# Kernel tuning notes

Hardware: AMD Instinct MI355X
Metric: run time of the kernel (lower is better)

Reference implementation:

```python
import jax, jax.numpy as jnp
import numpy as np

L, B, S, D, H, F, E, G, KG, K = 2, 2, 1024, 1024, 16, 1024, 8, 4, 2, 2
EPS = 1e-5
HD = D // H


def setup_inputs() -> dict:
    key = jax.random.key(0)
    ks = jax.random.split(key, 16)
    def nrm(k, shape):
        return jax.random.normal(k, shape, jnp.float32) * 0.02
    inp = {
        'src': jax.random.normal(ks[0], (B, S, D), jnp.float32),
        'attn_qkv_w': nrm(ks[1], (L, 3 * D, D)), 'attn_qkv_b': jnp.zeros((L, 3 * D), jnp.float32),
        'attn_out_w': nrm(ks[2], (L, D, D)), 'attn_out_b': jnp.zeros((L, D), jnp.float32),
        'norm1_g': jnp.ones((L, D), jnp.float32), 'norm1_b': jnp.zeros((L, D), jnp.float32),
        'norm2_g': jnp.ones((L, D), jnp.float32), 'norm2_b': jnp.zeros((L, D), jnp.float32),
        'gate_w': nrm(ks[3], (L, E, D)),
        'exp_w1': nrm(ks[4], (L, E, F, D)), 'exp_b1': jnp.zeros((L, E, F), jnp.float32),
        'exp_w2': nrm(ks[5], (L, E, D, F)), 'exp_b2': jnp.zeros((L, E, D), jnp.float32),
        'exp_w3': nrm(ks[6], (L, E, F, D)), 'exp_b3': jnp.zeros((L, E, F), jnp.float32),
        'sh_w1': nrm(ks[7], (L, F, D)), 'sh_b1': jnp.zeros((L, F), jnp.float32),
        'sh_w2': nrm(ks[8], (L, D, F)), 'sh_b2': jnp.zeros((L, D), jnp.float32),
        'sh_w3': nrm(ks[9], (L, F, D)), 'sh_b3': jnp.zeros((L, F), jnp.float32),
        'final_g': jnp.ones((D,), jnp.float32), 'final_b': jnp.zeros((D,), jnp.float32),
    }
    return inp


def _ln(x, g, b):
    mu = jnp.mean(x, -1, keepdims=True)
    var = jnp.mean(jnp.square(x - mu), -1, keepdims=True)
    return (x - mu) * jax.lax.rsqrt(var + EPS) * g + b


def _swiglu(x, w1, b1, w2, b2, w3, b3):
    return (jax.nn.silu(x @ w1.T + b1) * (x @ w3.T + b3)) @ w2.T + b2


def _attn(h, wqkv, bqkv, wo, bo):
    qkv = h @ wqkv.T + bqkv                       # (B,S,3D)
    q, k, v = jnp.split(qkv, 3, axis=-1)
    sp = lambda t: t.reshape(B, S, H, HD).transpose(0, 2, 1, 3)
    q, k, v = sp(q), sp(k), sp(v)
    sc = jnp.einsum('bhqd,bhkd->bhqk', q, k) / np.sqrt(HD).astype(np.float32)
    causal = jnp.tril(jnp.ones((S, S), bool))
    sc = jnp.where(causal, sc, -jnp.inf)
    a = jax.nn.softmax(sc, axis=-1)
    o = jnp.einsum('bhqk,bhkd->bhqd', a, v).transpose(0, 2, 1, 3).reshape(B, S, D)
    return o @ wo.T + bo


def _moe(x, gw, w1, b1, w2, b2, w3, b3, sw1, sb1, sw2, sb2, sw3, sb3):
    # x: (T,D) flattened tokens
    T = x.shape[0]
    scores = jax.nn.softmax(x @ gw.T, axis=-1)    # (T,E)
    orig = scores
    gs = scores.reshape(T, G, E // G)
    grp = gs.max(-1)                              # (T,G) group score = amax (bias is None)
    _, gidx = jax.lax.top_k(grp, KG)
    rows = jnp.arange(T)[:, None]
    gmask = jnp.zeros((T, G), bool).at[rows, gidx].set(True)
    masked = jnp.where(gmask[:, :, None], gs, -jnp.inf).reshape(T, E)
    _, idx = jax.lax.top_k(masked, K)             # (T,K) selected experts
    w = jnp.take_along_axis(orig, idx, axis=-1)   # (T,K) weights from original softmax scores
    comb = jnp.zeros((T, E), x.dtype).at[rows, idx].add(w)  # (T,E) combine weights
    outs = jax.vmap(lambda a, b_, c, d_, e, f: _swiglu(x, a, b_, c, d_, e, f))(w1, b1, w2, b2, w3, b3)  # (E,T,D)
    y = jnp.einsum('te,etd->td', comb, outs)
    z = _swiglu(x, sw1, sb1, sw2, sb2, sw3, sb3)  # shared expert
    return y + z


def reference(src, attn_qkv_w, attn_qkv_b, attn_out_w, attn_out_b,
              norm1_g, norm1_b, norm2_g, norm2_b, gate_w,
              exp_w1, exp_b1, exp_w2, exp_b2, exp_w3, exp_b3,
              sh_w1, sh_b1, sh_w2, sh_b2, sh_w3, sh_b3,
              final_g, final_b):
    y = src
    for l in range(L):
        h = _ln(y, norm1_g[l], norm1_b[l])
        y = y + _attn(h, attn_qkv_w[l], attn_qkv_b[l], attn_out_w[l], attn_out_b[l])
        h2 = _ln(y, norm2_g[l], norm2_b[l]).reshape(-1, D)
        ff = _moe(h2, gate_w[l],
                  exp_w1[l], exp_b1[l], exp_w2[l], exp_b2[l], exp_w3[l], exp_b3[l],
                  sh_w1[l], sh_b1[l], sh_w2[l], sh_b2[l], sh_w3[l], sh_b3[l])
        y = y + ff.reshape(B, S, D)
    return _ln(y, final_g, final_b)
```

## Files before the change

### kernel.cpp

```cpp
#include <hip/hip_runtime.h>
#include <cstdint>
#include <cstddef>

typedef __bf16 bf16_t;
typedef __attribute__((ext_vector_type(8))) __bf16 bf16x8;
typedef __attribute__((ext_vector_type(4))) float f32x4;

#define B_ 2
#define S_ 1024
#define D_ 1024
#define H_ 16
#define T_ 2048
#define E_ 8
#define F_ 1024
#define MOE_ROWS 5120
#define MAX_TILES 40

__device__ __forceinline__ void global_to_lds16(const void* g, void* l) {
  __builtin_amdgcn_global_load_lds(
      (__attribute__((address_space(1))) unsigned int*)(uintptr_t)g,
      (__attribute__((address_space(3))) unsigned int*)(unsigned int)(uintptr_t)l,
      16, 0, 0);
}

__device__ __forceinline__ void split2(float x, bf16_t& h, bf16_t& l) {
  h = (bf16_t)x;
  l = (bf16_t)(x - (float)h);
}

__global__ __launch_bounds__(256) void k_cvt2(const float* __restrict__ s,
    bf16_t* __restrict__ dh, bf16_t* __restrict__ dl, int n) {
  int i = (blockIdx.x * 256 + threadIdx.x) * 4;
  if (i >= n) return;
  float4 v = *(const float4*)(s + i);
  union { bf16_t h[4]; ushort4 u; } ch, cl;
  split2(v.x, ch.h[0], cl.h[0]);
  split2(v.y, ch.h[1], cl.h[1]);
  split2(v.z, ch.h[2], cl.h[2]);
  split2(v.w, ch.h[3], cl.h[3]);
  *(ushort4*)(dh + i) = ch.u;
  *(ushort4*)(dl + i) = cl.u;
}

__global__ __launch_bounds__(256) void k_cvt2s(const float* __restrict__ s,
    bf16_t* __restrict__ dh, bf16_t* __restrict__ dl, int n, int dstoff) {
  int i = (blockIdx.x * 256 + threadIdx.x) * 4;
  if (i >= n) return;
  int e = i >> 20;
  int r = i & 1048575;
  size_t di = (size_t)e * 2097152 + dstoff + r;
  float4 v = *(const float4*)(s + i);
  union { bf16_t h[4]; ushort4 u; } ch, cl;
  split2(v.x, ch.h[0], cl.h[0]);
  split2(v.y, ch.h[1], cl.h[1]);
  split2(v.z, ch.h[2], cl.h[2]);
  split2(v.w, ch.h[3], cl.h[3]);
  *(ushort4*)(dh + di) = ch.u;
  *(ushort4*)(dl + di) = cl.u;
}

__global__ __launch_bounds__(256) void k_catbias_e(const float* __restrict__ b1,
    const float* __restrict__ b3, float* __restrict__ d) {
  int i = blockIdx.x * 256 + threadIdx.x;
  int e = i >> 11, j = i & 2047;
  d[i] = (j < 1024) ? b1[e * 1024 + j] : b3[e * 1024 + j - 1024];
}

__global__ __launch_bounds__(256) void k_catbias_s(const float* __restrict__ b1,
    const float* __restrict__ b3, float* __restrict__ d) {
  int i = blockIdx.x * 256 + threadIdx.x;
  d[i] = (i < 1024) ? b1[i] : b3[i - 1024];
}

__global__ __launch_bounds__(256) void k_ln(const float* __restrict__ x,
    const float* __restrict__ g, const float* __restrict__ b,
    float* __restrict__ of, bf16_t* __restrict__ obh, bf16_t* __restrict__ obl) {
  int t = blockIdx.x, tid = threadIdx.x;
  const float4* xr = (const float4*)(x + (size_t)t * D_);
  float4 v = xr[tid];
  float s = v.x + v.y + v.z + v.w;
  float s2 = v.x * v.x + v.y * v.y + v.z * v.z + v.w * v.w;
#pragma unroll
  for (int o = 32; o; o >>= 1) { s += __shfl_xor(s, o, 64); s2 += __shfl_xor(s2, o, 64); }
  __shared__ float rs[4], rs2[4];
  if ((tid & 63) == 0) { rs[tid >> 6] = s; rs2[tid >> 6] = s2; }
  __syncthreads();
  s = rs[0] + rs[1] + rs[2] + rs[3];
  s2 = rs2[0] + rs2[1] + rs2[2] + rs2[3];
  float mu = s * (1.f / D_);
  float var = s2 * (1.f / D_) - mu * mu;
  float r = rsqrtf(var + 1e-5f);
  float4 gg = ((const float4*)g)[tid];
  float4 bb = ((const float4*)b)[tid];
  float4 o;
  o.x = (v.x - mu) * r * gg.x + bb.x;
  o.y = (v.y - mu) * r * gg.y + bb.y;
  o.z = (v.z - mu) * r * gg.z + bb.z;
  o.w = (v.w - mu) * r * gg.w + bb.w;
  if (of) ((float4*)(of + (size_t)t * D_))[tid] = o;
  if (obh) {
    union { bf16_t h[4]; ushort4 u; } ch, cl;
    split2(o.x, ch.h[0], cl.h[0]);
    split2(o.y, ch.h[1], cl.h[1]);
    split2(o.z, ch.h[2], cl.h[2]);
    split2(o.w, ch.h[3], cl.h[3]);
    *(ushort4*)(obh + (size_t)t * D_ + tid * 4) = ch.u;
    *(ushort4*)(obl + (size_t)t * D_ + tid * 4) = cl.u;
  }
}

__global__ __launch_bounds__(256) void k_gemm(const bf16_t* __restrict__ Ah,
    const bf16_t* __restrict__ Al, const bf16_t* __restrict__ Bh,
    const bf16_t* __restrict__ Bl, float* __restrict__ C,
    const float* __restrict__ bias, int M, int N, int K, int addC) {
  __shared__ __align__(16) bf16_t Ash[128 * 32];
  __shared__ __align__(16) bf16_t Asl[128 * 32];
  __shared__ __align__(16) bf16_t Bsh[128 * 32];
  __shared__ __align__(16) bf16_t Bsl[128 * 32];
  const int tid = threadIdx.x;
  const int wave = tid >> 6, lane = tid & 63;
  const int wm = (wave >> 1) << 6, wn = (wave & 1) << 6;
  const int lr = lane & 15, kg = lane >> 4;
  const int row0 = blockIdx.y * 128, col0 = blockIdx.x * 128;
  f32x4 acc[4][4] = {};
  for (int k0 = 0; k0 < K; k0 += 32) {
#pragma unroll
    for (int c = 0; c < 2; c++) {
      int o = c * 4096 + tid * 16;
      int r = o >> 6, cb = (o & 63) >> 1;
      size_t ga = (size_t)(row0 + r) * K + k0 + cb;
      size_t gb = (size_t)(col0 + r) * K + k0 + cb;
      global_to_lds16(Ah + ga, (char*)Ash + o);
      global_to_lds16(Al + ga, (char*)Asl + o);
      global_to_lds16(Bh + gb, (char*)Bsh + o);
      global_to_lds16(Bl + gb, (char*)Bsl + o);
    }
    __syncthreads();
    bf16x8 ah[4], al[4], bh[4], bl[4];
#pragma unroll
    for (int i = 0; i < 4; i++) {
      int ra = (wm + i * 16 + lr) * 32 + kg * 8;
      int rb = (wn + i * 16 + lr) * 32 + kg * 8;
      ah[i] = *(const bf16x8*)&Ash[ra];
      al[i] = *(const bf16x8*)&Asl[ra];
      bh[i] = *(const bf16x8*)&Bsh[rb];
      bl[i] = *(const bf16x8*)&Bsl[rb];
    }
#pragma unroll
    for (int mi = 0; mi < 4; mi++)
#pragma unroll
      for (int ni = 0; ni < 4; ni++) {
        acc[mi][ni] = __builtin_amdgcn_mfma_f32_16x16x32_bf16(ah[mi], bh[ni], acc[mi][ni], 0, 0, 0);
        acc[mi][ni] = __builtin_amdgcn_mfma_f32_16x16x32_bf16(ah[mi], bl[ni], acc[mi][ni], 0, 0, 0);
        acc[mi][ni] = __builtin_amdgcn_mfma_f32_16x16x32_bf16(al[mi], bh[ni], acc[mi][ni], 0, 0, 0);
      }
    __syncthreads();
  }
#pragma unroll
  for (int mi = 0; mi < 4; mi++) {
#pragma unroll
    for (int r = 0; r < 4; r++) {
      int m = row0 + wm + mi * 16 + kg * 4 + r;
      if (m >= M) continue;
      float* crow = C + (size_t)m * N;
#pragma unroll
      for (int ni = 0; ni < 4; ni++) {
        int n = col0 + wn + ni * 16 + lr;
        float v = acc[mi][ni][r];
        if (bias) v += bias[n];
        if (addC) crow[n] += v; else crow[n] = v;
      }
    }
  }
}

__global__ __launch_bounds__(256) void k_gemm_grp(const bf16_t* __restrict__ Ah,
    const bf16_t* __restrict__ Al, const bf16_t* __restrict__ Bbh,
    const bf16_t* __restrict__ Bbl, float* __restrict__ C,
    const float* __restrict__ biasbase,
    const int* __restrict__ tile_e, const int* __restrict__ tile_r0,
    const int* __restrict__ tile_rend, const int* __restrict__ ntl,
    int N, int K) {
  __shared__ __align__(16) bf16_t Ash[128 * 32];
  __shared__ __align__(16) bf16_t Asl[128 * 32];
  __shared__ __align__(16) bf16_t Bsh[128 * 32];
  __shared__ __align__(16) bf16_t Bsl[128 * 32];
  int ti = blockIdx.y;
  if (ti >= *ntl) return;
  const int e = tile_e[ti];
  const int row0 = tile_r0[ti];
  const int rend = tile_rend[ti];
  const bf16_t* Bh = Bbh + (size_t)e * N * K;
  const bf16_t* Bl = Bbl + (size_t)e * N * K;
  const float* bias = biasbase + (size_t)e * N;
  const int tid = threadIdx.x;
  const int wave = tid >> 6, lane = tid & 63;
  const int wm = (wave >> 1) << 6, wn = (wave & 1) << 6;
  const int lr = lane & 15, kg = lane >> 4;
  const int col0 = blockIdx.x * 128;
  f32x4 acc[4][4] = {};
  for (int k0 = 0; k0 < K; k0 += 32) {
#pragma unroll
    for (int c = 0; c < 2; c++) {
      int o = c * 4096 + tid * 16;
      int r = o >> 6, cb = (o & 63) >> 1;
      size_t ga = (size_t)(row0 + r) * K + k0 + cb;
      size_t gb = (size_t)(col0 + r) * K + k0 + cb;
      global_to_lds16(Ah + ga, (char*)Ash + o);
      global_to_lds16(Al + ga, (char*)Asl + o);
      global_to_lds16(Bh + gb, (char*)Bsh + o);
      global_to_lds16(Bl + gb, (char*)Bsl + o);
    }
    __syncthreads();
    bf16x8 ah[4], al[4], bh[4], bl[4];
#pragma unroll
    for (int i = 0; i < 4; i++) {
      int ra = (wm + i * 16 + lr) * 32 + kg * 8;
      int rb = (wn + i * 16 + lr) * 32 + kg * 8;
      ah[i] = *(const bf16x8*)&Ash[ra];
      al[i] = *(const bf16x8*)&Asl[ra];
      bh[i] = *(const bf16x8*)&Bsh[rb];
      bl[i] = *(const bf16x8*)&Bsl[rb];
    }
#pragma unroll
    for (int mi = 0; mi < 4; mi++)
#pragma unroll
      for (int ni = 0; ni < 4; ni++) {
        acc[mi][ni] = __builtin_amdgcn_mfma_f32_16x16x32_bf16(ah[mi], bh[ni], acc[mi][ni], 0, 0, 0);
        acc[mi][ni] = __builtin_amdgcn_mfma_f32_16x16x32_bf16(ah[mi], bl[ni], acc[mi][ni], 0, 0, 0);
        acc[mi][ni] = __builtin_amdgcn_mfma_f32_16x16x32_bf16(al[mi], bh[ni], acc[mi][ni], 0, 0, 0);
      }
    __syncthreads();
  }
#pragma unroll
  for (int mi = 0; mi < 4; mi++) {
#pragma unroll
    for (int r = 0; r < 4; r++) {
      int m = row0 + wm + mi * 16 + kg * 4 + r;
      if (m >= rend) continue;
      float* crow = C + (size_t)m * N;
#pragma unroll
      for (int ni = 0; ni < 4; ni++) {
        int n = col0 + wn + ni * 16 + lr;
        crow[n] = acc[mi][ni][r] + bias[n];
      }
    }
  }
}

__global__ __launch_bounds__(256) void k_attn(const float* __restrict__ qkv,
    bf16_t* __restrict__ ctxh, bf16_t* __restrict__ ctxl) {
  int blk = blockIdx.x;
  int qt = blk & 15, h = (blk >> 4) & 15, b = blk >> 8;
  int tid = threadIdx.x, wave = tid >> 6, lane = tid & 63;
  int lr = lane & 15, kg = lane >> 4;

  __shared__ __align__(16) bf16_t Ksh[64 * 72], Ksl[64 * 72];
  __shared__ __align__(16) bf16_t Vth[64 * 72], Vtl[64 * 72];
  __shared__ __align__(16) bf16_t Ph[4][16 * 72], Pl[4][16 * 72];

  int qrow = qt * 64 + wave * 16 + lr;
  const float* qptr = qkv + (size_t)(b * S_ + qrow) * 3072 + h * 64;
  bf16x8 qh[2], ql[2];
#pragma unroll
  for (int g = 0; g < 2; g++) {
    float4 v0 = *(const float4*)(qptr + g * 32 + kg * 8);
    float4 v1 = *(const float4*)(qptr + g * 32 + kg * 8 + 4);
    float f[8] = {v0.x, v0.y, v0.z, v0.w, v1.x, v1.y, v1.z, v1.w};
#pragma unroll
    for (int j = 0; j < 8; j++) {
      float x = f[j] * 0.125f;
      bf16_t hh = (bf16_t)x;
      qh[g][j] = hh;
      ql[g][j] = (bf16_t)(x - (float)hh);
    }
  }

  f32x4 acc[4] = {};
  float mrow[4], lrow[4];
#pragma unroll
  for (int r = 0; r < 4; r++) { mrow[r] = -1e30f; lrow[r] = 0.f; }

  for (int kt = 0; kt <= qt; kt++) {
    __syncthreads();
    {
      int row = tid >> 2;
      int c0 = (tid & 3) * 16;
      const float* kr = qkv + (size_t)(b * S_ + kt * 64 + row) * 3072 + 1024 + h * 64 + c0;
      const float* vr = kr + 1024;
#pragma unroll
      for (int cc = 0; cc < 16; cc += 4) {
        float4 kv = *(const float4*)(kr + cc);
        float4 vv = *(const float4*)(vr + cc);
        float kf[4] = {kv.x, kv.y, kv.z, kv.w};
        float vf[4] = {vv.x, vv.y, vv.z, vv.w};
#pragma unroll
        for (int u = 0; u < 4; u++) {
          int c = c0 + cc + u;
          bf16_t hh = (bf16_t)kf[u];
          Ksh[row * 72 + c] = hh;
          Ksl[row * 72 + c] = (bf16_t)(kf[u] - (float)hh);
          bf16_t vh = (bf16_t)vf[u];
          Vth[c * 72 + row] = vh;
          Vtl[c * 72 + row] = (bf16_t)(vf[u] - (float)vh);
        }
      }
    }
    __syncthreads();

    f32x4 sc[4];
#pragma unroll
    for (int ni = 0; ni < 4; ni++) {
      f32x4 s = {};
#pragma unroll
      for (int g = 0; g < 2; g++) {
        int ro = (ni * 16 + lr) * 72 + g * 32 + kg * 8;
        bf16x8 kh = *(const bf16x8*)&Ksh[ro];
        bf16x8 kl = *(const bf16x8*)&Ksl[ro];
        s = __builtin_amdgcn_mfma_f32_16x16x32_bf16(qh[g], kh, s, 0, 0, 0);
        s = __builtin_amdgcn_mfma_f32_16x16x32_bf16(qh[g], kl, s, 0, 0, 0);
        s = __builtin_amdgcn_mfma_f32_16x16x32_bf16(ql[g], kh, s, 0, 0, 0);
      }
      sc[ni] = s;
    }

    int kbase = kt * 64;
    int myrow = qt * 64 + wave * 16 + kg * 4;
    if (kt == qt) {
#pragma unroll
      for (int ni = 0; ni < 4; ni++)
#pragma unroll
        for (int r = 0; r < 4; r++)
          if (kbase + ni * 16 + lr > myrow + r) sc[ni][r] = -1e30f;
    }

    float alpha[4];
#pragma unroll
    for (int r = 0; r < 4; r++) {
      float v = fmaxf(fmaxf(sc[0][r], sc[1][r]), fmaxf(sc[2][r], sc[3][r]));
#pragma unroll
      for (int o = 8; o; o >>= 1) v = fmaxf(v, __shfl_xor(v, o, 64));
      float mn = fmaxf(mrow[r], v);
      alpha[r] = __expf(mrow[r] - mn);
      mrow[r] = mn;
    }
    float rsum[4] = {0.f, 0.f, 0.f, 0.f};
#pragma unroll
    for (int ni = 0; ni < 4; ni++) {
#pragma unroll
      for (int r = 0; r < 4; r++) {
        float p = __expf(sc[ni][r] - mrow[r]);
        rsum[r] += p;
        bf16_t ph = (bf16_t)p;
        int po_ = (kg * 4 + r) * 72 + ni * 16 + lr;
        Ph[wave][po_] = ph;
        Pl[wave][po_] = (bf16_t)(p - (float)ph);
      }
    }
#pragma unroll
    for (int r = 0; r < 4; r++) {
      float v = rsum[r];
#pragma unroll
      for (int o = 8; o; o >>= 1) v += __shfl_xor(v, o, 64);
      lrow[r] = lrow[r] * alpha[r] + v;
    }
#pragma unroll
    for (int ni = 0; ni < 4; ni++)
#pragma unroll
      for (int r = 0; r < 4; r++) acc[ni][r] *= alpha[r];

    bf16x8 pfh[2], pfl[2];
#pragma unroll
    for (int g = 0; g < 2; g++) {
      int po_ = lr * 72 + g * 32 + kg * 8;
      pfh[g] = *(const bf16x8*)&Ph[wave][po_];
      pfl[g] = *(const bf16x8*)&Pl[wave][po_];
    }
#pragma unroll
    for (int ni = 0; ni < 4; ni++) {
#pragma unroll
      for (int g = 0; g < 2; g++) {
        int vo = (ni * 16 + lr) * 72 + g * 32 + kg * 8;
        bf16x8 vh = *(const bf16x8*)&Vth[vo];
        bf16x8 vl = *(const bf16x8*)&Vtl[vo];
        acc[ni] = __builtin_amdgcn_mfma_f32_16x16x32_bf16(pfh[g], vh, acc[ni], 0, 0, 0);
        acc[ni] = __builtin_amdgcn_mfma_f32_16x16x32_bf16(pfh[g], vl, acc[ni], 0, 0, 0);
        acc[ni] = __builtin_amdgcn_mfma_f32_16x16x32_bf16(pfl[g], vh, acc[ni], 0, 0, 0);
      }
    }
  }

  int trow = b * S_ + qt * 64 + wave * 16 + kg * 4;
#pragma unroll
  for (int r = 0; r < 4; r++) {
    float inv = 1.f / lrow[r];
#pragma unroll
    for (int ni = 0; ni < 4; ni++) {
      float x = acc[ni][r] * inv;
      bf16_t hh = (bf16_t)x;
      size_t idx = (size_t)(trow + r) * D_ + h * 64 + ni * 16 + lr;
      ctxh[idx] = hh;
      ctxl[idx] = (bf16_t)(x - (float)hh);
    }
  }
}

__global__ __launch_bounds__(64) void k_route(const float* __restrict__ h2,
    const float* __restrict__ gw, int* __restrict__ eidx, float* __restrict__ ew,
    int* __restrict__ cnt) {
  int t = blockIdx.x, lane = threadIdx.x;
  const float* x = h2 + (size_t)t * D_;
  float lg[8];
#pragma unroll
  for (int e = 0; e < 8; e++) {
    const float* w = gw + e * D_;
    float a = 0.f;
    for (int d = lane; d < D_; d += 64) a += x[d] * w[d];
#pragma unroll
    for (int o = 32; o; o >>= 1) a += __shfl_xor(a, o, 64);
    lg[e] = a;
  }
  if (lane == 0) {
    float mx = lg[0];
    for (int e = 1; e < 8; e++) mx = fmaxf(mx, lg[e]);
    float p[8], sum = 0.f;
    for (int e = 0; e < 8; e++) { p[e] = __expf(lg[e] - mx); sum += p[e]; }
    float inv = 1.f / sum;
    for (int e = 0; e < 8; e++) p[e] *= inv;
    float gs[4];
    for (int gi = 0; gi < 4; gi++) gs[gi] = fmaxf(p[2 * gi], p[2 * gi + 1]);
    int g0 = 0;
    for (int gi = 1; gi < 4; gi++) if (gs[gi] > gs[g0]) g0 = gi;
    int g1 = -1;
    for (int gi = 0; gi < 4; gi++) {
      if (gi == g0) continue;
      if (g1 < 0 || gs[gi] > gs[g1]) g1 = gi;
    }
    int i0 = -1, i1 = -1; float v0 = -1.f, v1 = -1.f;
    for (int e = 0; e < 8; e++) {
      int gi = e >> 1;
      if (gi != g0 && gi != g1) continue;
      if (p[e] > v0) { v1 = v0; i1 = i0; v0 = p[e]; i0 = e; }
      else if (p[e] > v1) { v1 = p[e]; i1 = e; }
    }
    eidx[2 * t] = i0; eidx[2 * t + 1] = i1;
    ew[2 * t] = v0; ew[2 * t + 1] = v1;
    atomicAdd(&cnt[i0], 1);
    atomicAdd(&cnt[i1], 1);
  }
}

__global__ void k_offsets(const int* __restrict__ cnt, int* __restrict__ poff,
                          int* __restrict__ te, int* __restrict__ tr0,
                          int* __restrict__ trend, int* __restrict__ ntl) {
  if (threadIdx.x != 0 || blockIdx.x != 0) return;
  int offv = 0, nt = 0;
  for (int e = 0; e < 8; e++) {
    poff[e] = offv;
    int c = cnt[e];
    int ntile = (c + 127) >> 7;
    for (int i = 0; i < ntile; i++) {
      te[nt] = e; tr0[nt] = offv + i * 128; trend[nt] = offv + c; nt++;
    }
    offv += ntile << 7;
  }
  poff[8] = offv;
  *ntl = nt;
}

__global__ __launch_bounds__(256) void k_fill(const int* __restrict__ eidx,
    const int* __restrict__ poff,
    int* __restrict__ cur, int* __restrict__ rowtok, int* __restrict__ postk) {
  int t = blockIdx.x * 256 + threadIdx.x;
  if (t >= T_) return;
#pragma unroll
  for (int k = 0; k < 2; k++) {
    int e = eidx[2 * t + k];
    int r = atomicAdd(&cur[e], 1);
    int pos = poff[e] + r;
    rowtok[pos] = t;
    postk[2 * t + k] = pos;
  }
}

__global__ __launch_bounds__(256) void k_gather(const int* __restrict__ rowtok,
    const bf16_t* __restrict__ h2h, const bf16_t* __restrict__ h2l,
    bf16_t* __restrict__ amh, bf16_t* __restrict__ aml) {
  int rrow = blockIdx.x;
  int tid = threadIdx.x;
  int t = rowtok[rrow];
  ushort4* dh = (ushort4*)(amh + (size_t)rrow * D_);
  ushort4* dl = (ushort4*)(aml + (size_t)rrow * D_);
  if (t < 0) {
    dh[tid] = make_ushort4(0, 0, 0, 0);
    dl[tid] = make_ushort4(0, 0, 0, 0);
  } else {
    dh[tid] = ((const ushort4*)(h2h + (size_t)t * D_))[tid];
    dl[tid] = ((const ushort4*)(h2l + (size_t)t * D_))[tid];
  }
}

__global__ __launch_bounds__(256) void k_swiglu2(const float* __restrict__ h13,
    bf16_t* __restrict__ acth, bf16_t* __restrict__ actl) {
  int row = blockIdx.x, tid = threadIdx.x;
  const float4* hr = (const float4*)(h13 + (size_t)row * 2048);
  float4 a = hr[tid];
  float4 c = hr[256 + tid];
  float4 o;
  o.x = a.x / (1.f + __expf(-a.x)) * c.x;
  o.y = a.y / (1.f + __expf(-a.y)) * c.y;
  o.z = a.z / (1.f + __expf(-a.z)) * c.z;
  o.w = a.w / (1.f + __expf(-a.w)) * c.w;
  union { bf16_t h[4]; ushort4 u; } ch, cl;
  split2(o.x, ch.h[0], cl.h[0]);
  split2(o.y, ch.h[1], cl.h[1]);
  split2(o.z, ch.h[2], cl.h[2]);
  split2(o.w, ch.h[3], cl.h[3]);
  ((ushort4*)acth)[(size_t)row * 256 + tid] = ch.u;
  ((ushort4*)actl)[(size_t)row * 256 + tid] = cl.u;
}

__global__ __launch_bounds__(256) void k_scatter(const float* __restrict__ outm,
    const int* __restrict__ postk, const float* __restrict__ ewt,
    float* __restrict__ y) {
  int t = blockIdx.x, tid = threadIdx.x;
  int p0 = postk[2 * t], p1 = postk[2 * t + 1];
  float w0 = ewt[2 * t], w1 = ewt[2 * t + 1];
  float4* yr = (float4*)(y + (size_t)t * D_);
  const float4* a = (const float4*)(outm + (size_t)p0 * D_);
  const float4* b = (const float4*)(outm + (size_t)p1 * D_);
  float4 v = yr[tid], va = a[tid], vb = b[tid];
  v.x += w0 * va.x + w1 * vb.x;
  v.y += w0 * va.y + w1 * vb.y;
  v.z += w0 * va.z + w1 * vb.z;
  v.w += w0 * va.w + w1 * vb.w;
  yr[tid] = v;
}

extern "C" void kernel_launch(void* const* d_in, const int* in_sizes, int n_in,
                              void* d_out, int out_size, void* d_ws, size_t ws_size,
                              hipStream_t stream) {
  const float* src  = (const float*)d_in[0];
  const float* qkvw = (const float*)d_in[1];
  const float* qkvb = (const float*)d_in[2];
  const float* outw = (const float*)d_in[3];
  const float* outb = (const float*)d_in[4];
  const float* n1g  = (const float*)d_in[5];
  const float* n1b  = (const float*)d_in[6];
  const float* n2g  = (const float*)d_in[7];
  const float* n2b  = (const float*)d_in[8];
  const float* gw   = (const float*)d_in[9];
  const float* ew1  = (const float*)d_in[10];
  const float* eb1  = (const float*)d_in[11];
  const float* ew2  = (const float*)d_in[12];
  const float* eb2  = (const float*)d_in[13];
  const float* ew3  = (const float*)d_in[14];
  const float* eb3  = (const float*)d_in[15];
  const float* sw1  = (const float*)d_in[16];
  const float* sb1  = (const float*)d_in[17];
  const float* sw2  = (const float*)d_in[18];
  const float* sb2  = (const float*)d_in[19];
  const float* sw3  = (const float*)d_in[20];
  const float* sb3  = (const float*)d_in[21];
  const float* fng  = (const float*)d_in[22];
  const float* fnb  = (const float*)d_in[23];
  float* outp = (float*)d_out;

  char* base = (char*)d_ws;
  size_t off = 0;
  auto alloc = [&](size_t bytes) -> void* {
    off = (off + 255) & ~(size_t)255;
    void* r = base + off;
    off += bytes;
    return r;
  };
  bf16_t* wqkv_h  = (bf16_t*)alloc((size_t)3072 * 1024 * 2);
  bf16_t* wqkv_l  = (bf16_t*)alloc((size_t)3072 * 1024 * 2);
  bf16_t* wout_h  = (bf16_t*)alloc((size_t)1024 * 1024 * 2);
  bf16_t* wout_l  = (bf16_t*)alloc((size_t)1024 * 1024 * 2);
  bf16_t* we13_h  = (bf16_t*)alloc((size_t)16 * 1024 * 1024 * 2);
  bf16_t* we13_l  = (bf16_t*)alloc((size_t)16 * 1024 * 1024 * 2);
  bf16_t* we2_h   = (bf16_t*)alloc((size_t)8 * 1024 * 1024 * 2);
  bf16_t* we2_l   = (bf16_t*)alloc((size_t)8 * 1024 * 1024 * 2);
  bf16_t* wsh13_h = (bf16_t*)alloc((size_t)2 * 1024 * 1024 * 2);
  bf16_t* wsh13_l = (bf16_t*)alloc((size_t)2 * 1024 * 1024 * 2);
  bf16_t* wsh2_h  = (bf16_t*)alloc((size_t)1024 * 1024 * 2);
  bf16_t* wsh2_l  = (bf16_t*)alloc((size_t)1024 * 1024 * 2);
  float*  ebc13   = (float*)alloc((size_t)8 * 2048 * 4);
  float*  sbc13   = (float*)alloc((size_t)2048 * 4);
  float*  y    = (float*)alloc((size_t)T_ * D_ * 4);
  float*  lnf  = (float*)alloc((size_t)T_ * D_ * 4);
  bf16_t* lnb_h = (bf16_t*)alloc((size_t)T_ * D_ * 2);
  bf16_t* lnb_l = (bf16_t*)alloc((size_t)T_ * D_ * 2);
  bf16_t* ctx_h = (bf16_t*)alloc((size_t)T_ * D_ * 2);
  bf16_t* ctx_l = (bf16_t*)alloc((size_t)T_ * D_ * 2);
  char* regA   = (char*)alloc((size_t)MOE_ROWS * 2048 * 4);
  float* qkvbuf = (float*)regA;
  float* h13m   = (float*)regA;
  float* outm   = (float*)regA;
  float* h13s   = (float*)regA;
  char* regU = (char*)alloc((size_t)4 * MOE_ROWS * 1024 * 2);
  bf16_t* act_h  = (bf16_t*)regU;
  bf16_t* act_l  = (bf16_t*)(regU + (size_t)MOE_ROWS * 1024 * 2);
  bf16_t* amoe_h = (bf16_t*)(regU + (size_t)2 * MOE_ROWS * 1024 * 2);
  bf16_t* amoe_l = (bf16_t*)(regU + (size_t)3 * MOE_ROWS * 1024 * 2);
  int*   eidx = (int*)alloc((size_t)T_ * 2 * 4);
  float* ewt  = (float*)alloc((size_t)T_ * 2 * 4);
  int* cnt  = (int*)alloc(64);
  int* cur  = (int*)alloc(64);
  int* poff = (int*)alloc(64);
  int* te   = (int*)alloc(256);
  int* tr0  = (int*)alloc(256);
  int* trend = (int*)alloc(256);
  int* ntl  = (int*)alloc(16);
  int* rowtok = (int*)alloc((size_t)MOE_ROWS * 4);
  int* postk  = (int*)alloc((size_t)T_ * 2 * 4);
  (void)ws_size; (void)in_sizes; (void)n_in; (void)out_size;

  (void)hipMemcpyAsync(y, src, (size_t)T_ * D_ * 4, hipMemcpyDeviceToDevice, stream);

  for (int l = 0; l < 2; l++) {
    size_t lf = (size_t)l;
    k_cvt2<<<3072, 256, 0, stream>>>(qkvw + lf * 3145728, wqkv_h, wqkv_l, 3145728);
    k_cvt2<<<1024, 256, 0, stream>>>(outw + lf * 1048576, wout_h, wout_l, 1048576);
    k_cvt2s<<<8192, 256, 0, stream>>>(ew1 + lf * 8388608, we13_h, we13_l, 8388608, 0);
    k_cvt2s<<<8192, 256, 0, stream>>>(ew3 + lf * 8388608, we13_h, we13_l, 8388608, 1048576);
    k_cvt2<<<8192, 256, 0, stream>>>(ew2 + lf * 8388608, we2_h, we2_l, 8388608);
    k_cvt2<<<1024, 256, 0, stream>>>(sw1 + lf * 1048576, wsh13_h, wsh13_l, 1048576);
    k_cvt2<<<1024, 256, 0, stream>>>(sw3 + lf * 1048576, wsh13_h + 1048576, wsh13_l + 1048576, 1048576);
    k_cvt2<<<1024, 256, 0, stream>>>(sw2 + lf * 1048576, wsh2_h, wsh2_l, 1048576);
    k_catbias_e<<<64, 256, 0, stream>>>(eb1 + lf * 8192, eb3 + lf * 8192, ebc13);
    k_catbias_s<<<8, 256, 0, stream>>>(sb1 + lf * 1024, sb3 + lf * 1024, sbc13);

    k_ln<<<T_, 256, 0, stream>>>(y, n1g + lf * 1024, n1b + lf * 1024,
                                 (float*)nullptr, lnb_h, lnb_l);
    k_gemm<<<dim3(24, 16), 256, 0, stream>>>(lnb_h, lnb_l, wqkv_h, wqkv_l, qkvbuf,
                                             qkvb + lf * 3072, T_, 3072, 1024, 0);
    k_attn<<<512, 256, 0, stream>>>(qkvbuf, ctx_h, ctx_l);
    k_gemm<<<dim3(8, 16), 256, 0, stream>>>(ctx_h, ctx_l, wout_h, wout_l, y,
                                            outb + lf * 1024, T_, 1024, 1024, 1);
    k_ln<<<T_, 256, 0, stream>>>(y, n2g + lf * 1024, n2b + lf * 1024, lnf, lnb_h, lnb_l);

    (void)hipMemsetAsync(cnt, 0, 64, stream);
    (void)hipMemsetAsync(cur, 0, 64, stream);
    (void)hipMemsetAsync(rowtok, 0xFF, (size_t)MOE_ROWS * 4, stream);
    k_route<<<T_, 64, 0, stream>>>(lnf, gw + lf * 8192, eidx, ewt, cnt);
    k_offsets<<<1, 1, 0, stream>>>(cnt, poff, te, tr0, trend, ntl);
    k_fill<<<8, 256, 0, stream>>>(eidx, poff, cur, rowtok, postk);
    k_gather<<<MOE_ROWS, 256, 0, stream>>>(rowtok, lnb_h, lnb_l, amoe_h, amoe_l);

    k_gemm_grp<<<dim3(16, MAX_TILES), 256, 0, stream>>>(amoe_h, amoe_l, we13_h, we13_l,
        h13m, ebc13, te, tr0, trend, ntl, 2048, 1024);
    k_swiglu2<<<MOE_ROWS, 256, 0, stream>>>(h13m, act_h, act_l);
    k_gemm_grp<<<dim3(8, MAX_TILES), 256, 0, stream>>>(act_h, act_l, we2_h, we2_l, outm,
        eb2 + lf * 8192, te, tr0, trend, ntl, 1024, 1024);
    k_scatter<<<T_, 256, 0, stream>>>(outm, postk, ewt, y);

    k_gemm<<<dim3(16, 16), 256, 0, stream>>>(lnb_h, lnb_l, wsh13_h, wsh13_l, h13s,
                                             sbc13, T_, 2048, 1024, 0);
    k_swiglu2<<<T_, 256, 0, stream>>>(h13s, act_h, act_l);
    k_gemm<<<dim3(8, 16), 256, 0, stream>>>(act_h, act_l, wsh2_h, wsh2_l, y,
                                            sb2 + lf * 1024, T_, 1024, 1024, 1);
  }

  k_ln<<<T_, 256, 0, stream>>>(y, fng, fnb, outp, (bf16_t*)nullptr, (bf16_t*)nullptr);
}
```

Measured before the change: 1.612 ms.

## Fuse SwiGLU into expert up-GEMM and fold shared expert into grouped MoE

```diff
diff --git a/kernel.cpp b/kernel.cpp
--- a/kernel.cpp
+++ b/kernel.cpp
@@ -13,8 +13,9 @@
 #define T_ 2048
 #define E_ 8
 #define F_ 1024
-#define MOE_ROWS 5120
-#define MAX_TILES 40
+#define RT_ROWS 5120
+#define ALL_ROWS 7168
+#define MAX_TILES 56
 
 __device__ __forceinline__ void global_to_lds16(const void* g, void* l) {
   __builtin_amdgcn_global_load_lds(
@@ -28,28 +29,10 @@
   l = (bf16_t)(x - (float)h);
 }
 
-__global__ __launch_bounds__(256) void k_cvt2(const float* __restrict__ s,
-    bf16_t* __restrict__ dh, bf16_t* __restrict__ dl, int n) {
-  int i = (blockIdx.x * 256 + threadIdx.x) * 4;
-  if (i >= n) return;
-  float4 v = *(const float4*)(s + i);
-  union { bf16_t h[4]; ushort4 u; } ch, cl;
-  split2(v.x, ch.h[0], cl.h[0]);
-  split2(v.y, ch.h[1], cl.h[1]);
-  split2(v.z, ch.h[2], cl.h[2]);
-  split2(v.w, ch.h[3], cl.h[3]);
-  *(ushort4*)(dh + i) = ch.u;
-  *(ushort4*)(dl + i) = cl.u;
-}
-
-__global__ __launch_bounds__(256) void k_cvt2s(const float* __restrict__ s,
-    bf16_t* __restrict__ dh, bf16_t* __restrict__ dl, int n, int dstoff) {
-  int i = (blockIdx.x * 256 + threadIdx.x) * 4;
-  if (i >= n) return;
-  int e = i >> 20;
-  int r = i & 1048575;
-  size_t di = (size_t)e * 2097152 + dstoff + r;
-  float4 v = *(const float4*)(s + i);
+__device__ __forceinline__ void cvt4(const float* __restrict__ s, size_t si,
+                                     bf16_t* __restrict__ dh, bf16_t* __restrict__ dl,
+                                     size_t di) {
+  float4 v = *(const float4*)(s + si);
   union { bf16_t h[4]; ushort4 u; } ch, cl;
   split2(v.x, ch.h[0], cl.h[0]);
   split2(v.y, ch.h[1], cl.h[1]);
@@ -59,17 +42,69 @@
   *(ushort4*)(dl + di) = cl.u;
 }
 
-__global__ __launch_bounds__(256) void k_catbias_e(const float* __restrict__ b1,
-    const float* __restrict__ b3, float* __restrict__ d) {
+__global__ __launch_bounds__(256) void k_cvtall(
+    const float* __restrict__ qkvw, const float* __restrict__ outw,
+    const float* __restrict__ ew1, const float* __restrict__ ew3,
+    const float* __restrict__ ew2, const float* __restrict__ sw1,
+    const float* __restrict__ sw3, const float* __restrict__ sw2,
+    bf16_t* __restrict__ wqkv_h, bf16_t* __restrict__ wqkv_l,
+    bf16_t* __restrict__ wout_h, bf16_t* __restrict__ wout_l,
+    bf16_t* __restrict__ we13_h, bf16_t* __restrict__ we13_l,
+    bf16_t* __restrict__ we2_h,  bf16_t* __restrict__ we2_l,
+    int* __restrict__ cnt, int* __restrict__ cur) {
+  int blk = blockIdx.x;
+  if (blk == 0 && threadIdx.x < 16) {
+    if (threadIdx.x < 8) cnt[threadIdx.x] = 0;
+    else cur[threadIdx.x - 8] = 0;
+  }
+  if (blk < 3072) {
+    size_t i = (size_t)blk * 1024 + threadIdx.x * 4;
+    cvt4(qkvw, i, wqkv_h, wqkv_l, i);
+  } else if (blk < 4096) {
+    size_t i = (size_t)(blk - 3072) * 1024 + threadIdx.x * 4;
+    cvt4(outw, i, wout_h, wout_l, i);
+  } else if (blk < 12288) {
+    size_t i = (size_t)(blk - 4096) * 1024 + threadIdx.x * 4;
+    size_t e = i >> 20, r = i & 1048575;
+    cvt4(ew1, i, we13_h, we13_l, e * 2097152 + ((r >> 10) << 11) + (r & 1023));
+  } else if (blk < 20480) {
+    size_t i = (size_t)(blk - 12288) * 1024 + threadIdx.x * 4;
+    size_t e = i >> 20, r = i & 1048575;
+    cvt4(ew3, i, we13_h, we13_l, e * 2097152 + ((r >> 10) << 11) + 1024 + (r & 1023));
+  } else if (blk < 28672) {
+    size_t i = (size_t)(blk - 20480) * 1024 + threadIdx.x * 4;
+    cvt4(ew2, i, we2_h, we2_l, i);
+  } else if (blk < 29696) {
+    size_t i = (size_t)(blk - 28672) * 1024 + threadIdx.x * 4;
+    cvt4(sw1, i, we13_h, we13_l, (size_t)8 * 2097152 + ((i >> 10) << 11) + (i & 1023));
+  } else if (blk < 30720) {
+    size_t i = (size_t)(blk - 29696) * 1024 + threadIdx.x * 4;
+    cvt4(sw3, i, we13_h, we13_l, (size_t)8 * 2097152 + ((i >> 10) << 11) + 1024 + (i & 1023));
+  } else {
+    size_t i = (size_t)(blk - 30720) * 1024 + threadIdx.x * 4;
+    cvt4(sw2, i, we2_h, we2_l, (size_t)8 * 1048576 + i);
+  }
+}
+
+__global__ __launch_bounds__(256) void k_catbias(const float* __restrict__ eb1,
+    const float* __restrict__ eb3, const float* __restrict__ sb1,
+    const float* __restrict__ sb3, const float* __restrict__ eb2,
+    const float* __restrict__ sb2, float* __restrict__ ebc13,
+    float* __restrict__ eb2c) {
   int i = blockIdx.x * 256 + threadIdx.x;
-  int e = i >> 11, j = i & 2047;
-  d[i] = (j < 1024) ? b1[e * 1024 + j] : b3[e * 1024 + j - 1024];
-}
-
-__global__ __launch_bounds__(256) void k_catbias_s(const float* __restrict__ b1,
-    const float* __restrict__ b3, float* __restrict__ d) {
-  int i = blockIdx.x * 256 + threadIdx.x;
-  d[i] = (i < 1024) ? b1[i] : b3[i - 1024];
+  if (i < 9 * 2048) {
+    int e = i >> 11, c = i & 2047, j = c >> 1;
+    float v;
+    if (e < 8) v = ((c & 1) == 0) ? eb1[e * 1024 + j] : eb3[e * 1024 + j];
+    else       v = ((c & 1) == 0) ? sb1[j] : sb3[j];
+    ebc13[i] = v;
+  } else {
+    int k = i - 9 * 2048;
+    if (k < 9 * 1024) {
+      int e = k >> 10, j = k & 1023;
+      eb2c[k] = (e < 8) ? eb2[e * 1024 + j] : sb2[j];
+    }
+  }
 }
 
 __global__ __launch_bounds__(256) void k_ln(const float* __restrict__ x,
@@ -169,6 +204,91 @@
         float v = acc[mi][ni][r];
         if (bias) v += bias[n];
         if (addC) crow[n] += v; else crow[n] = v;
+      }
+    }
+  }
+}
+
+__global__ __launch_bounds__(256) void k_gemm_up(const bf16_t* __restrict__ Ah,
+    const bf16_t* __restrict__ Al, const bf16_t* __restrict__ Sh,
+    const bf16_t* __restrict__ Sl, const bf16_t* __restrict__ Bbh,
+    const bf16_t* __restrict__ Bbl, bf16_t* __restrict__ acth,
+    bf16_t* __restrict__ actl, const float* __restrict__ biasbase,
+    const int* __restrict__ tile_e, const int* __restrict__ tile_r0,
+    const int* __restrict__ tile_rend, const int* __restrict__ ntl) {
+  __shared__ __align__(16) bf16_t Ash[128 * 32];
+  __shared__ __align__(16) bf16_t Asl[128 * 32];
+  __shared__ __align__(16) bf16_t Bsh[128 * 32];
+  __shared__ __align__(16) bf16_t Bsl[128 * 32];
+  const int K = 1024;
+  int ti = blockIdx.y;
+  if (ti >= *ntl) return;
+  const int e = tile_e[ti];
+  const int row0 = tile_r0[ti];
+  const int rend = tile_rend[ti];
+  const bf16_t* Abh = (e < 8) ? Ah + (size_t)row0 * K : Sh + (size_t)(row0 - RT_ROWS) * K;
+  const bf16_t* Abl = (e < 8) ? Al + (size_t)row0 * K : Sl + (size_t)(row0 - RT_ROWS) * K;
+  const bf16_t* Bh = Bbh + (size_t)e * 2048 * K;
+  const bf16_t* Bl = Bbl + (size_t)e * 2048 * K;
+  const float* bias = biasbase + (size_t)e * 2048;
+  const int tid = threadIdx.x;
+  const int wave = tid >> 6, lane = tid & 63;
+  const int wm = (wave >> 1) << 6, wn = (wave & 1) << 6;
+  const int lr = lane & 15, kg = lane >> 4;
+  const int col0 = blockIdx.x * 128;
+  f32x4 acc[4][4] = {};
+  for (int k0 = 0; k0 < K; k0 += 32) {
+#pragma unroll
+    for (int c = 0; c < 2; c++) {
+      int o = c * 4096 + tid * 16;
+      int r = o >> 6, cb = (o & 63) >> 1;
+      size_t ga = (size_t)r * K + k0 + cb;
+      size_t gb = (size_t)(col0 + r) * K + k0 + cb;
+      global_to_lds16(Abh + ga, (char*)Ash + o);
+      global_to_lds16(Abl + ga, (char*)Asl + o);
+      global_to_lds16(Bh + gb, (char*)Bsh + o);
+      global_to_lds16(Bl + gb, (char*)Bsl + o);
+    }
+    __syncthreads();
+    bf16x8 ah[4], al[4], bh[4], bl[4];
+#pragma unroll
+    for (int i = 0; i < 4; i++) {
+      int ra = (wm + i * 16 + lr) * 32 + kg * 8;
+      int rb = (wn + i * 16 + lr) * 32 + kg * 8;
+      ah[i] = *(const bf16x8*)&Ash[ra];
+      al[i] = *(const bf16x8*)&Asl[ra];
+      bh[i] = *(const bf16x8*)&Bsh[rb];
+      bl[i] = *(const bf16x8*)&Bsl[rb];
+    }
+#pragma unroll
+    for (int mi = 0; mi < 4; mi++)
+#pragma unroll
+      for (int ni = 0; ni < 4; ni++) {
+        acc[mi][ni] = __builtin_amdgcn_mfma_f32_16x16x32_bf16(ah[mi], bh[ni], acc[mi][ni], 0, 0, 0);
+        acc[mi][ni] = __builtin_amdgcn_mfma_f32_16x16x32_bf16(ah[mi], bl[ni], acc[mi][ni], 0, 0, 0);
+        acc[mi][ni] = __builtin_amdgcn_mfma_f32_16x16x32_bf16(al[mi], bh[ni], acc[mi][ni], 0, 0, 0);
+      }
+    __syncthreads();
+  }
+#pragma unroll
+  for (int mi = 0; mi < 4; mi++) {
+#pragma unroll
+    for (int r = 0; r < 4; r++) {
+      int m = row0 + wm + mi * 16 + kg * 4 + r;
+      bool ok = (m < rend);
+#pragma unroll
+      for (int ni = 0; ni < 4; ni++) {
+        int col = col0 + wn + ni * 16 + lr;
+        float v = acc[mi][ni][r] + bias[col];
+        float p = __shfl_xor(v, 1, 64);
+        if (ok && !(lane & 1)) {
+          float o = v / (1.f + __expf(-v)) * p;
+          bf16_t hh, ll;
+          split2(o, hh, ll);
+          size_t di = (size_t)m * 1024 + (col >> 1);
+          acth[di] = hh;
+          actl[di] = ll;
+        }
       }
     }
   }
@@ -450,10 +570,11 @@
   }
 }
 
-__global__ void k_offsets(const int* __restrict__ cnt, int* __restrict__ poff,
-                          int* __restrict__ te, int* __restrict__ tr0,
-                          int* __restrict__ trend, int* __restrict__ ntl) {
-  if (threadIdx.x != 0 || blockIdx.x != 0) return;
+__global__ __launch_bounds__(256) void k_offsets(const int* __restrict__ cnt,
+    int* __restrict__ poff, int* __restrict__ te, int* __restrict__ tr0,
+    int* __restrict__ trend, int* __restrict__ ntl, int* __restrict__ rowtok) {
+  for (int i = threadIdx.x; i < RT_ROWS; i += 256) rowtok[i] = -1;
+  if (threadIdx.x != 0) return;
   int offv = 0, nt = 0;
   for (int e = 0; e < 8; e++) {
     poff[e] = offv;
@@ -465,6 +586,9 @@
     offv += ntile << 7;
   }
   poff[8] = offv;
+  for (int i = 0; i < 16; i++) {
+    te[nt] = 8; tr0[nt] = RT_ROWS + i * 128; trend[nt] = ALL_ROWS; nt++;
+  }
   *ntl = nt;
 }
 
@@ -500,26 +624,6 @@
   }
 }
 
-__global__ __launch_bounds__(256) void k_swiglu2(const float* __restrict__ h13,
-    bf16_t* __restrict__ acth, bf16_t* __restrict__ actl) {
-  int row = blockIdx.x, tid = threadIdx.x;
-  const float4* hr = (const float4*)(h13 + (size_t)row * 2048);
-  float4 a = hr[tid];
-  float4 c = hr[256 + tid];
-  float4 o;
-  o.x = a.x / (1.f + __expf(-a.x)) * c.x;
-  o.y = a.y / (1.f + __expf(-a.y)) * c.y;
-  o.z = a.z / (1.f + __expf(-a.z)) * c.z;
-  o.w = a.w / (1.f + __expf(-a.w)) * c.w;
-  union { bf16_t h[4]; ushort4 u; } ch, cl;
-  split2(o.x, ch.h[0], cl.h[0]);
-  split2(o.y, ch.h[1], cl.h[1]);
-  split2(o.z, ch.h[2], cl.h[2]);
-  split2(o.w, ch.h[3], cl.h[3]);
-  ((ushort4*)acth)[(size_t)row * 256 + tid] = ch.u;
-  ((ushort4*)actl)[(size_t)row * 256 + tid] = cl.u;
-}
-
 __global__ __launch_bounds__(256) void k_scatter(const float* __restrict__ outm,
     const int* __restrict__ postk, const float* __restrict__ ewt,
     float* __restrict__ y) {
@@ -529,11 +633,12 @@
   float4* yr = (float4*)(y + (size_t)t * D_);
   const float4* a = (const float4*)(outm + (size_t)p0 * D_);
   const float4* b = (const float4*)(outm + (size_t)p1 * D_);
-  float4 v = yr[tid], va = a[tid], vb = b[tid];
-  v.x += w0 * va.x + w1 * vb.x;
-  v.y += w0 * va.y + w1 * vb.y;
-  v.z += w0 * va.z + w1 * vb.z;
-  v.w += w0 * va.w + w1 * vb.w;
+  const float4* s = (const float4*)(outm + (size_t)(RT_ROWS + t) * D_);
+  float4 v = yr[tid], va = a[tid], vb = b[tid], vs = s[tid];
+  v.x += w0 * va.x + w1 * vb.x + vs.x;
+  v.y += w0 * va.y + w1 * vb.y + vs.y;
+  v.z += w0 * va.z + w1 * vb.z + vs.z;
+  v.w += w0 * va.w + w1 * vb.w + vs.w;
   yr[tid] = v;
 }
 
@@ -578,32 +683,25 @@
   bf16_t* wqkv_l  = (bf16_t*)alloc((size_t)3072 * 1024 * 2);
   bf16_t* wout_h  = (bf16_t*)alloc((size_t)1024 * 1024 * 2);
   bf16_t* wout_l  = (bf16_t*)alloc((size_t)1024 * 1024 * 2);
-  bf16_t* we13_h  = (bf16_t*)alloc((size_t)16 * 1024 * 1024 * 2);
-  bf16_t* we13_l  = (bf16_t*)alloc((size_t)16 * 1024 * 1024 * 2);
-  bf16_t* we2_h   = (bf16_t*)alloc((size_t)8 * 1024 * 1024 * 2);
-  bf16_t* we2_l   = (bf16_t*)alloc((size_t)8 * 1024 * 1024 * 2);
-  bf16_t* wsh13_h = (bf16_t*)alloc((size_t)2 * 1024 * 1024 * 2);
-  bf16_t* wsh13_l = (bf16_t*)alloc((size_t)2 * 1024 * 1024 * 2);
-  bf16_t* wsh2_h  = (bf16_t*)alloc((size_t)1024 * 1024 * 2);
-  bf16_t* wsh2_l  = (bf16_t*)alloc((size_t)1024 * 1024 * 2);
-  float*  ebc13   = (float*)alloc((size_t)8 * 2048 * 4);
-  float*  sbc13   = (float*)alloc((size_t)2048 * 4);
+  bf16_t* we13_h  = (bf16_t*)alloc((size_t)9 * 2048 * 1024 * 2);
+  bf16_t* we13_l  = (bf16_t*)alloc((size_t)9 * 2048 * 1024 * 2);
+  bf16_t* we2_h   = (bf16_t*)alloc((size_t)9 * 1024 * 1024 * 2);
+  bf16_t* we2_l   = (bf16_t*)alloc((size_t)9 * 1024 * 1024 * 2);
+  float*  ebc13   = (float*)alloc((size_t)9 * 2048 * 4);
+  float*  eb2c    = (float*)alloc((size_t)9 * 1024 * 4);
   float*  y    = (float*)alloc((size_t)T_ * D_ * 4);
   float*  lnf  = (float*)alloc((size_t)T_ * D_ * 4);
   bf16_t* lnb_h = (bf16_t*)alloc((size_t)T_ * D_ * 2);
   bf16_t* lnb_l = (bf16_t*)alloc((size_t)T_ * D_ * 2);
   bf16_t* ctx_h = (bf16_t*)alloc((size_t)T_ * D_ * 2);
   bf16_t* ctx_l = (bf16_t*)alloc((size_t)T_ * D_ * 2);
-  char* regA   = (char*)alloc((size_t)MOE_ROWS * 2048 * 4);
+  char* regA   = (char*)alloc((size_t)ALL_ROWS * 1024 * 4);
   float* qkvbuf = (float*)regA;
-  float* h13m   = (float*)regA;
   float* outm   = (float*)regA;
-  float* h13s   = (float*)regA;
-  char* regU = (char*)alloc((size_t)4 * MOE_ROWS * 1024 * 2);
-  bf16_t* act_h  = (bf16_t*)regU;
-  bf16_t* act_l  = (bf16_t*)(regU + (size_t)MOE_ROWS * 1024 * 2);
-  bf16_t* amoe_h = (bf16_t*)(regU + (size_t)2 * MOE_ROWS * 1024 * 2);
-  bf16_t* amoe_l = (bf16_t*)(regU + (size_t)3 * MOE_ROWS * 1024 * 2);
+  bf16_t* act_h  = (bf16_t*)alloc((size_t)ALL_ROWS * 1024 * 2);
+  bf16_t* act_l  = (bf16_t*)alloc((size_t)ALL_ROWS * 1024 * 2);
+  bf16_t* amoe_h = (bf16_t*)alloc((size_t)RT_ROWS * 1024 * 2);
+  bf16_t* amoe_l = (bf16_t*)alloc((size_t)RT_ROWS * 1024 * 2);
   int*   eidx = (int*)alloc((size_t)T_ * 2 * 4);
   float* ewt  = (float*)alloc((size_t)T_ * 2 * 4);
   int* cnt  = (int*)alloc(64);
@@ -613,7 +711,7 @@
   int* tr0  = (int*)alloc(256);
   int* trend = (int*)alloc(256);
   int* ntl  = (int*)alloc(16);
-  int* rowtok = (int*)alloc((size_t)MOE_ROWS * 4);
+  int* rowtok = (int*)alloc((size_t)RT_ROWS * 4);
   int* postk  = (int*)alloc((size_t)T_ * 2 * 4);
   (void)ws_size; (void)in_sizes; (void)n_in; (void)out_size;
 
@@ -621,16 +719,14 @@
 
   for (int l = 0; l < 2; l++) {
     size_t lf = (size_t)l;
-    k_cvt2<<<3072, 256, 0, stream>>>(qkvw + lf * 3145728, wqkv_h, wqkv_l, 3145728);
-    k_cvt2<<<1024, 256, 0, stream>>>(outw + lf * 1048576, wout_h, wout_l, 1048576);
-    k_cvt2s<<<8192, 256, 0, stream>>>(ew1 + lf * 8388608, we13_h, we13_l, 8388608, 0);
-    k_cvt2s<<<8192, 256, 0, stream>>>(ew3 + lf * 8388608, we13_h, we13_l, 8388608, 1048576);
-    k_cvt2<<<8192, 256, 0, stream>>>(ew2 + lf * 8388608, we2_h, we2_l, 8388608);
-    k_cvt2<<<1024, 256, 0, stream>>>(sw1 + lf * 1048576, wsh13_h, wsh13_l, 1048576);
-    k_cvt2<<<1024, 256, 0, stream>>>(sw3 + lf * 1048576, wsh13_h + 1048576, wsh13_l + 1048576, 1048576);
-    k_cvt2<<<1024, 256, 0, stream>>>(sw2 + lf * 1048576, wsh2_h, wsh2_l, 1048576);
-    k_catbias_e<<<64, 256, 0, stream>>>(eb1 + lf * 8192, eb3 + lf * 8192, ebc13);
-    k_catbias_s<<<8, 256, 0, stream>>>(sb1 + lf * 1024, sb3 + lf * 1024, sbc13);
+    k_cvtall<<<31744, 256, 0, stream>>>(
+        qkvw + lf * 3145728, outw + lf * 1048576,
+        ew1 + lf * 8388608, ew3 + lf * 8388608, ew2 + lf * 8388608,
+        sw1 + lf * 1048576, sw3 + lf * 1048576, sw2 + lf * 1048576,
+        wqkv_h, wqkv_l, wout_h, wout_l, we13_h, we13_l, we2_h, we2_l, cnt, cur);
+    k_catbias<<<108, 256, 0, stream>>>(eb1 + lf * 8192, eb3 + lf * 8192,
+        sb1 + lf * 1024, sb3 + lf * 1024, eb2 + lf * 8192, sb2 + lf * 1024,
+        ebc13, eb2c);
 
     k_ln<<<T_, 256, 0, stream>>>(y, n1g + lf * 1024, n1b + lf * 1024,
                                  (float*)nullptr, lnb_h, lnb_l);
@@ -641,26 +737,16 @@
                                             outb + lf * 1024, T_, 1024, 1024, 1);
     k_ln<<<T_, 256, 0, stream>>>(y, n2g + lf * 1024, n2b + lf * 1024, lnf, lnb_h, lnb_l);
 
-    (void)hipMemsetAsync(cnt, 0, 64, stream);
-    (void)hipMemsetAsync(cur, 0, 64, stream);
-    (void)hipMemsetAsync(rowtok, 0xFF, (size_t)MOE_ROWS * 4, stream);
     k_route<<<T_, 64, 0, stream>>>(lnf, gw + lf * 8192, eidx, ewt, cnt);
-    k_offsets<<<1, 1, 0, stream>>>(cnt, poff, te, tr0, trend, ntl);
+    k_offsets<<<1, 256, 0, stream>>>(cnt, poff, te, tr0, trend, ntl, rowtok);
     k_fill<<<8, 256, 0, stream>>>(eidx, poff, cur, rowtok, postk);
-    k_gather<<<MOE_ROWS, 256, 0, stream>>>(rowtok, lnb_h, lnb_l, amoe_h, amoe_l);
-
-    k_gemm_grp<<<dim3(16, MAX_TILES), 256, 0, stream>>>(amoe_h, amoe_l, we13_h, we13_l,
-        h13m, ebc13, te, tr0, trend, ntl, 2048, 1024);
-    k_swiglu2<<<MOE_ROWS, 256, 0, stream>>>(h13m, act_h, act_l);
+    k_gather<<<RT_ROWS, 256, 0, stream>>>(rowtok, lnb_h, lnb_l, amoe_h, amoe_l);
+
+    k_gemm_up<<<dim3(16, MAX_TILES), 256, 0, stream>>>(amoe_h, amoe_l, lnb_h, lnb_l,
+        we13_h, we13_l, act_h, act_l, ebc13, te, tr0, trend, ntl);
     k_gemm_grp<<<dim3(8, MAX_TILES), 256, 0, stream>>>(act_h, act_l, we2_h, we2_l, outm,
-        eb2 + lf * 8192, te, tr0, trend, ntl, 1024, 1024);
+        eb2c, te, tr0, trend, ntl, 1024, 1024);
     k_scatter<<<T_, 256, 0, stream>>>(outm, postk, ewt, y);
-
-    k_gemm<<<dim3(16, 16), 256, 0, stream>>>(lnb_h, lnb_l, wsh13_h, wsh13_l, h13s,
-                                             sbc13, T_, 2048, 1024, 0);
-    k_swiglu2<<<T_, 256, 0, stream>>>(h13s, act_h, act_l);
-    k_gemm<<<dim3(8, 16), 256, 0, stream>>>(act_h, act_l, wsh2_h, wsh2_l, y,
-                                            sb2 + lf * 1024, T_, 1024, 1024, 1);
   }
 
   k_ln<<<T_, 256, 0, stream>>>(y, fng, fnb, outp, (bf16_t*)nullptr, (bf16_t*)nullptr);
```

New measurement: 1.331 ms. -17.4%, faster.
